# Performance work log

Hardware: AMD Instinct MI355X
Metric: run time of the kernel (lower is better)

## Reference

```python
import jax, jax.numpy as jnp
import numpy as np

N_NODES = 50000
N_EDGES = 800000
D_FEAT = 100


def setup_inputs() -> dict:
    key = jax.random.key(0)
    ks = jax.random.split(key, 10)
    s = 0.1
    x = jax.random.normal(ks[0], (N_NODES, D_FEAT), dtype=jnp.float32)
    edge_index = jax.random.randint(ks[1], (2, N_EDGES), 0, N_NODES, dtype=jnp.int32)
    return {
        "x": x,
        "edge_index": edge_index,
        "convW0": jax.random.normal(ks[2], (100, 100), jnp.float32) * s,
        "convb0": jnp.zeros((100,), jnp.float32),
        "convW1": jax.random.normal(ks[3], (100, 100), jnp.float32) * s,
        "convb1": jnp.zeros((100,), jnp.float32),
        "linW0": jax.random.normal(ks[4], (100, 10), jnp.float32) * s,
        "linb0": jnp.zeros((10,), jnp.float32),
        "linW1": jax.random.normal(ks[5], (10, 1), jnp.float32) * s,
        "linb1": jnp.zeros((1,), jnp.float32),
    }


def _gcn_conv(x, W, b, src, dst, n):
    """PyG GCNConv: h = x @ W; out[i] = sum_{(j->i)} d_j^{-1/2} d_i^{-1/2} h[j] + b,
    with self-loops already included in (src, dst)."""
    h = x @ W  # [N, out]
    deg = jax.ops.segment_sum(jnp.ones(src.shape[0], x.dtype), dst, num_segments=n)
    dinv = jnp.where(deg > 0, jax.lax.rsqrt(deg), jnp.zeros_like(deg))
    norm = dinv[src] * dinv[dst]  # [E_tot]
    msg = norm[:, None] * h[src]  # gather [E_tot, out]
    out = jax.ops.segment_sum(msg, dst, num_segments=n)  # scatter-add
    return out + b


def reference(x, edge_index, convW0, convb0, convW1, convb1, linW0, linb0, linW1, linb1):
    n = x.shape[0]
    # global-norm division (x.div(torch.norm(x).detach()))
    nm = jax.lax.stop_gradient(jnp.linalg.norm(x))
    x = x / nm
    # NOTE: original re-assigns x via sklearn SelectKBest(chi2, k=100) on raw data.x;
    # that is non-differentiable data preprocessing, so we assume x already holds the
    # k=100 selected features.
    loops = jnp.arange(n, dtype=edge_index.dtype)
    src = jnp.concatenate([edge_index[0], loops])  # self-loops appended
    dst = jnp.concatenate([edge_index[1], loops])
    x = _gcn_conv(x, convW0, convb0, src, dst, n)
    x = _gcn_conv(x, convW1, convb1, src, dst, n)
    # MLP head: ReLU between layers, no activation after the last (loop breaks)
    x = jax.nn.relu(x @ linW0 + linb0)
    x = x @ linW1 + linb1
    return x.T  # [1, N]
```

## Files before the change

kernel.cpp:

```cpp
#include <hip/hip_runtime.h>

#define NN 50000
#define NE 800000
#define ELLW 64
#define CSTR 16

__device__ __forceinline__ float wredf(float v) {
    #pragma unroll
    for (int o = 32; o > 0; o >>= 1) v += __shfl_down(v, o, 64);
    return v;
}

__global__ __launch_bounds__(256) void k_fill(
    const int* __restrict__ src, const int* __restrict__ dst,
    int* __restrict__ curp, int* __restrict__ ell,
    const float* __restrict__ W0, const float* __restrict__ W1,
    const float* __restrict__ cb0, const float* __restrict__ cb1,
    const float* __restrict__ L0, const float* __restrict__ lb0,
    float* __restrict__ Wz, float* __restrict__ uvec, float* __restrict__ cvec)
{
    int b = blockIdx.x, t = threadIdx.x;
    if (b < 3125) {
        int e = b * 256 + t;
        int s = src[e];
        int d = dst[e];
        int p = atomicAdd(&curp[d * CSTR], 1);
        if (p < ELLW) ell[d * ELLW + p] = s;
        return;
    }
    __shared__ float WA[1000];
    for (int o = t; o < 1000; o += 256) {
        int j = o / 10, m = o % 10;
        float s = 0.f;
        for (int k = 0; k < 100; ++k) s += W1[j * 100 + k] * L0[k * 10 + m];
        WA[o] = s;
    }
    __syncthreads();
    for (int o = t; o < 1000; o += 256) {
        int i = o / 10, m = o % 10;
        float s = 0.f;
        for (int k = 0; k < 100; ++k) s += W0[i * 100 + k] * WA[k * 10 + m];
        Wz[o] = s;
    }
    if (t < 10) {
        float su = 0.f, scv = 0.f;
        for (int k = 0; k < 100; ++k) {
            su  += cb0[k] * WA[k * 10 + t];
            scv += cb1[k] * L0[k * 10 + t];
        }
        uvec[t] = su;
        cvec[t] = scv + lb0[t];
    }
}

__global__ __launch_bounds__(256) void k_proj(
    const float* __restrict__ x, const float* __restrict__ Wz,
    const int* __restrict__ curp, float* __restrict__ acc,
    float* __restrict__ gp)
{
    __shared__ float w[1000];
    for (int o = threadIdx.x; o < 1000; o += 256) w[o] = Wz[o];
    __syncthreads();
    int i = blockIdx.x * 256 + threadIdx.x;
    float ss = 0.f;
    float h[10];
    #pragma unroll
    for (int m = 0; m < 10; ++m) h[m] = 0.f;
    if (i < NN) {
        const float4* r4 = (const float4*)(x + i * 100);
        for (int kk = 0; kk < 25; ++kk) {
            float4 a = r4[kk];
            ss += a.x * a.x + a.y * a.y + a.z * a.z + a.w * a.w;
            #pragma unroll
            for (int j = 0; j < 4; ++j) {
                float av = ((const float*)&a)[j];
                int k = kk * 4 + j;
                #pragma unroll
                for (int m = 0; m < 10; ++m) h[m] += av * w[k * 10 + m];
            }
        }
    }
    ss = wredf(ss);
    __shared__ float p[4];
    if ((threadIdx.x & 63) == 0) p[threadIdx.x >> 6] = ss;
    __syncthreads();
    if (threadIdx.x == 0) atomicAdd(acc, p[0] + p[1] + p[2] + p[3]);

    if (i < NN) {
        float dv = rsqrtf((float)(curp[i * CSTR] + 1));
        float o16[16];
        #pragma unroll
        for (int m = 0; m < 10; ++m) o16[m] = dv * h[m];
        o16[10] = dv;
        o16[11] = o16[12] = o16[13] = o16[14] = o16[15] = 0.f;
        float4* dst4 = (float4*)(gp + i * 16);
        #pragma unroll
        for (int q = 0; q < 4; ++q) dst4[q] = *(float4*)&o16[q * 4];
    } else if (i == NN) {
        float4 z = {0.f, 0.f, 0.f, 0.f};
        float4* d4 = (float4*)(gp + NN * 16);
        d4[0] = z; d4[1] = z; d4[2] = z; d4[3] = z;
    }
}

__global__ __launch_bounds__(256) void k_agg1(
    const float* __restrict__ gp, const int* __restrict__ curp,
    const int* __restrict__ ell, const float* __restrict__ acc,
    float* __restrict__ tb)
{
    int n = (blockIdx.x * 256 + threadIdx.x) >> 6;
    int l = threadIdx.x & 63, g = l >> 4, lane16 = l & 15;
    if (n > NN) return;
    if (n == NN) {
        if (l < 16) tb[NN * 16 + lane16] = 0.f;
        return;
    }
    int deg = curp[n * CSTR];
    int lim = min(deg, ELLW);
    float dvn = rsqrtf((float)(deg + 1));
    const int* rp = ell + n * ELLW;
    float a0 = (g == 0) ? gp[n * 16 + lane16] : 0.f;
    float a1 = 0.f, a2 = 0.f, a3 = 0.f;
    int nq = (lim + 3) >> 2;
    int k = g, q = 0;
    for (; q + 4 <= nq; q += 4, k += 16) {
        int i0 = (k      < lim) ? rp[k]      : NN;
        int i1 = (k + 4  < lim) ? rp[k + 4]  : NN;
        int i2 = (k + 8  < lim) ? rp[k + 8]  : NN;
        int i3 = (k + 12 < lim) ? rp[k + 12] : NN;
        a0 += gp[i0 * 16 + lane16];
        a1 += gp[i1 * 16 + lane16];
        a2 += gp[i2 * 16 + lane16];
        a3 += gp[i3 * 16 + lane16];
    }
    for (; q < nq; ++q, k += 4) {
        int i0 = (k < lim) ? rp[k] : NN;
        a0 += gp[i0 * 16 + lane16];
    }
    float s = (a0 + a1) + (a2 + a3);
    s += __shfl_xor(s, 16, 64);
    s += __shfl_xor(s, 32, 64);
    if (l < 16) {
        float sc = rsqrtf(*acc);
        float o = (lane16 < 10) ? sc * dvn * dvn * s
                                : (lane16 == 10 ? dvn * s : 0.f);
        tb[n * 16 + lane16] = o;
    }
}

__global__ __launch_bounds__(256) void k_agg2(
    const float* __restrict__ tb, const int* __restrict__ curp,
    const int* __restrict__ ell, const float* __restrict__ uvec,
    const float* __restrict__ cvec, const float* __restrict__ L1,
    const float* __restrict__ lb1, float* __restrict__ out)
{
    __shared__ float su[10], scv[10], sl[10];
    if (threadIdx.x < 10) {
        su[threadIdx.x]  = uvec[threadIdx.x];
        scv[threadIdx.x] = cvec[threadIdx.x];
        sl[threadIdx.x]  = L1[threadIdx.x];
    }
    __syncthreads();
    int n = (blockIdx.x * 256 + threadIdx.x) >> 6;
    int l = threadIdx.x & 63, g = l >> 4, lane16 = l & 15;
    int deg = curp[n * CSTR];
    int lim = min(deg, ELLW);
    float dvn = rsqrtf((float)(deg + 1));
    const int* rp = ell + n * ELLW;
    float a0 = (g == 0) ? tb[n * 16 + lane16] : 0.f;
    float a1 = 0.f, a2 = 0.f, a3 = 0.f;
    int nq = (lim + 3) >> 2;
    int k = g, q = 0;
    for (; q + 4 <= nq; q += 4, k += 16) {
        int i0 = (k      < lim) ? rp[k]      : NN;
        int i1 = (k + 4  < lim) ? rp[k + 4]  : NN;
        int i2 = (k + 8  < lim) ? rp[k + 8]  : NN;
        int i3 = (k + 12 < lim) ? rp[k + 12] : NN;
        a0 += tb[i0 * 16 + lane16];
        a1 += tb[i1 * 16 + lane16];
        a2 += tb[i2 * 16 + lane16];
        a3 += tb[i3 * 16 + lane16];
    }
    for (; q < nq; ++q, k += 4) {
        int i0 = (k < lim) ? rp[k] : NN;
        a0 += tb[i0 * 16 + lane16];
    }
    float s = (a0 + a1) + (a2 + a3);
    s += __shfl_xor(s, 16, 64);
    s += __shfl_xor(s, 32, 64);
    if (l < 16) {
        float v = tb[n * 16 + 10];
        float hidden = 0.f;
        if (lane16 < 10)
            hidden = fmaxf(dvn * s + v * su[lane16] + scv[lane16], 0.f) * sl[lane16];
        #pragma unroll
        for (int o = 8; o; o >>= 1) hidden += __shfl_down(hidden, o, 16);
        if (lane16 == 0) out[n] = hidden + lb1[0];
    }
}

extern "C" void kernel_launch(void* const* d_in, const int* in_sizes, int n_in,
                              void* d_out, int out_size, void* d_ws, size_t ws_size,
                              hipStream_t stream) {
    const float* x   = (const float*)d_in[0];
    const int*   ei  = (const int*)d_in[1];
    const int*   src = ei;
    const int*   dst = ei + NE;
    const float* W0  = (const float*)d_in[2];
    const float* cb0 = (const float*)d_in[3];
    const float* W1  = (const float*)d_in[4];
    const float* cb1 = (const float*)d_in[5];
    const float* lw0 = (const float*)d_in[6];
    const float* lb0 = (const float*)d_in[7];
    const float* lw1 = (const float*)d_in[8];
    const float* lb1 = (const float*)d_in[9];
    float* out = (float*)d_out;

    char* ws = (char*)d_ws;
    float* acc   = (float*)(ws + 0);
    int*   curp  = (int*)  (ws + 256);
    const size_t zspan = 3200384;
    float* Wz    = (float*)(ws + 3200384);
    float* uvec  = (float*)(ws + 3204480);
    float* cvec  = (float*)(ws + 3204608);
    int*   ell   = (int*)  (ws + 3204864);
    float* gp    = (float*)(ws + 16004864);
    float* tb    = (float*)(ws + 19204928);

    hipMemsetAsync(d_ws, 0, zspan, stream);
    k_fill <<<3126, 256, 0, stream>>>(src, dst, curp, ell,
                                      W0, W1, cb0, cb1, lw0, lb0, Wz, uvec, cvec);
    k_proj <<<196, 256, 0, stream>>>(x, Wz, curp, acc, gp);
    k_agg1 <<<12501, 256, 0, stream>>>(gp, curp, ell, acc, tb);
    k_agg2 <<<12500, 256, 0, stream>>>(tb, curp, ell, uvec, cvec, lw1, lb1, out);
}
```

Measured before the change: 211.2 us.

## Pack degree counters densely and broadcast ELL row via wave shuffles

Stores the per-node degree counters contiguously instead of padded at a 64-byte stride, which shrinks the memset span and the counter footprint read by later kernels. In both aggregation kernels each lane loads one ELL entry up front with a coalesced read, and neighbour indices are distributed with __shfl instead of repeated scattered loads from the row. The risk is more atomic contention on shared cache lines during the fill, plus extra cross-lane shuffle instructions.

```diff
diff --git a/kernel.cpp b/kernel.cpp
--- a/kernel.cpp
+++ b/kernel.cpp
@@ -3,7 +3,6 @@
 #define NN 50000
 #define NE 800000
 #define ELLW 64
-#define CSTR 16
 
 __device__ __forceinline__ float wredf(float v) {
     #pragma unroll
@@ -13,7 +12,7 @@
 
 __global__ __launch_bounds__(256) void k_fill(
     const int* __restrict__ src, const int* __restrict__ dst,
-    int* __restrict__ curp, int* __restrict__ ell,
+    int* __restrict__ cursor, int* __restrict__ ell,
     const float* __restrict__ W0, const float* __restrict__ W1,
     const float* __restrict__ cb0, const float* __restrict__ cb1,
     const float* __restrict__ L0, const float* __restrict__ lb0,
@@ -24,7 +23,7 @@
         int e = b * 256 + t;
         int s = src[e];
         int d = dst[e];
-        int p = atomicAdd(&curp[d * CSTR], 1);
+        int p = atomicAdd(&cursor[d], 1);
         if (p < ELLW) ell[d * ELLW + p] = s;
         return;
     }
@@ -55,7 +54,7 @@
 
 __global__ __launch_bounds__(256) void k_proj(
     const float* __restrict__ x, const float* __restrict__ Wz,
-    const int* __restrict__ curp, float* __restrict__ acc,
+    const int* __restrict__ cursor, float* __restrict__ acc,
     float* __restrict__ gp)
 {
     __shared__ float w[1000];
@@ -87,7 +86,7 @@
     if (threadIdx.x == 0) atomicAdd(acc, p[0] + p[1] + p[2] + p[3]);
 
     if (i < NN) {
-        float dv = rsqrtf((float)(curp[i * CSTR] + 1));
+        float dv = rsqrtf((float)(cursor[i] + 1));
         float o16[16];
         #pragma unroll
         for (int m = 0; m < 10; ++m) o16[m] = dv * h[m];
@@ -104,7 +103,7 @@
 }
 
 __global__ __launch_bounds__(256) void k_agg1(
-    const float* __restrict__ gp, const int* __restrict__ curp,
+    const float* __restrict__ gp, const int* __restrict__ cursor,
     const int* __restrict__ ell, const float* __restrict__ acc,
     float* __restrict__ tb)
 {
@@ -115,26 +114,33 @@
         if (l < 16) tb[NN * 16 + lane16] = 0.f;
         return;
     }
-    int deg = curp[n * CSTR];
+    int rpl = ell[n * ELLW + l];
+    int deg = cursor[n];
     int lim = min(deg, ELLW);
     float dvn = rsqrtf((float)(deg + 1));
-    const int* rp = ell + n * ELLW;
     float a0 = (g == 0) ? gp[n * 16 + lane16] : 0.f;
     float a1 = 0.f, a2 = 0.f, a3 = 0.f;
     int nq = (lim + 3) >> 2;
-    int k = g, q = 0;
-    for (; q + 4 <= nq; q += 4, k += 16) {
-        int i0 = (k      < lim) ? rp[k]      : NN;
-        int i1 = (k + 4  < lim) ? rp[k + 4]  : NN;
-        int i2 = (k + 8  < lim) ? rp[k + 8]  : NN;
-        int i3 = (k + 12 < lim) ? rp[k + 12] : NN;
+    int q = 0;
+    for (; q + 4 <= nq; q += 4) {
+        int s0 = 4 * q + g;
+        int v0 = __shfl(rpl, s0,      64);
+        int v1 = __shfl(rpl, s0 + 4,  64);
+        int v2 = __shfl(rpl, s0 + 8,  64);
+        int v3 = __shfl(rpl, s0 + 12, 64);
+        int i0 = (s0      < lim) ? v0 : NN;
+        int i1 = (s0 + 4  < lim) ? v1 : NN;
+        int i2 = (s0 + 8  < lim) ? v2 : NN;
+        int i3 = (s0 + 12 < lim) ? v3 : NN;
         a0 += gp[i0 * 16 + lane16];
         a1 += gp[i1 * 16 + lane16];
         a2 += gp[i2 * 16 + lane16];
         a3 += gp[i3 * 16 + lane16];
     }
-    for (; q < nq; ++q, k += 4) {
-        int i0 = (k < lim) ? rp[k] : NN;
+    for (; q < nq; ++q) {
+        int s0 = 4 * q + g;
+        int v0 = __shfl(rpl, s0, 64);
+        int i0 = (s0 < lim) ? v0 : NN;
         a0 += gp[i0 * 16 + lane16];
     }
     float s = (a0 + a1) + (a2 + a3);
@@ -149,7 +155,7 @@
 }
 
 __global__ __launch_bounds__(256) void k_agg2(
-    const float* __restrict__ tb, const int* __restrict__ curp,
+    const float* __restrict__ tb, const int* __restrict__ cursor,
     const int* __restrict__ ell, const float* __restrict__ uvec,
     const float* __restrict__ cvec, const float* __restrict__ L1,
     const float* __restrict__ lb1, float* __restrict__ out)
@@ -163,26 +169,33 @@
     __syncthreads();
     int n = (blockIdx.x * 256 + threadIdx.x) >> 6;
     int l = threadIdx.x & 63, g = l >> 4, lane16 = l & 15;
-    int deg = curp[n * CSTR];
+    int rpl = ell[n * ELLW + l];
+    int deg = cursor[n];
     int lim = min(deg, ELLW);
     float dvn = rsqrtf((float)(deg + 1));
-    const int* rp = ell + n * ELLW;
     float a0 = (g == 0) ? tb[n * 16 + lane16] : 0.f;
     float a1 = 0.f, a2 = 0.f, a3 = 0.f;
     int nq = (lim + 3) >> 2;
-    int k = g, q = 0;
-    for (; q + 4 <= nq; q += 4, k += 16) {
-        int i0 = (k      < lim) ? rp[k]      : NN;
-        int i1 = (k + 4  < lim) ? rp[k + 4]  : NN;
-        int i2 = (k + 8  < lim) ? rp[k + 8]  : NN;
-        int i3 = (k + 12 < lim) ? rp[k + 12] : NN;
+    int q = 0;
+    for (; q + 4 <= nq; q += 4) {
+        int s0 = 4 * q + g;
+        int v0 = __shfl(rpl, s0,      64);
+        int v1 = __shfl(rpl, s0 + 4,  64);
+        int v2 = __shfl(rpl, s0 + 8,  64);
+        int v3 = __shfl(rpl, s0 + 12, 64);
+        int i0 = (s0      < lim) ? v0 : NN;
+        int i1 = (s0 + 4  < lim) ? v1 : NN;
+        int i2 = (s0 + 8  < lim) ? v2 : NN;
+        int i3 = (s0 + 12 < lim) ? v3 : NN;
         a0 += tb[i0 * 16 + lane16];
         a1 += tb[i1 * 16 + lane16];
         a2 += tb[i2 * 16 + lane16];
         a3 += tb[i3 * 16 + lane16];
     }
-    for (; q < nq; ++q, k += 4) {
-        int i0 = (k < lim) ? rp[k] : NN;
+    for (; q < nq; ++q) {
+        int s0 = 4 * q + g;
+        int v0 = __shfl(rpl, s0, 64);
+        int i0 = (s0 < lim) ? v0 : NN;
         a0 += tb[i0 * 16 + lane16];
     }
     float s = (a0 + a1) + (a2 + a3);
@@ -218,19 +231,19 @@
 
     char* ws = (char*)d_ws;
     float* acc   = (float*)(ws + 0);
-    int*   curp  = (int*)  (ws + 256);
-    const size_t zspan = 3200384;
-    float* Wz    = (float*)(ws + 3200384);
-    float* uvec  = (float*)(ws + 3204480);
-    float* cvec  = (float*)(ws + 3204608);
-    int*   ell   = (int*)  (ws + 3204864);
-    float* gp    = (float*)(ws + 16004864);
-    float* tb    = (float*)(ws + 19204928);
+    int*   cursor= (int*)  (ws + 256);
+    const size_t zspan = 200320;
+    float* Wz    = (float*)(ws + 200448);
+    float* uvec  = (float*)(ws + 204544);
+    float* cvec  = (float*)(ws + 204672);
+    int*   ell   = (int*)  (ws + 204800);
+    float* gp    = (float*)(ws + 13004800);
+    float* tb    = (float*)(ws + 16204864);
 
     hipMemsetAsync(d_ws, 0, zspan, stream);
-    k_fill <<<3126, 256, 0, stream>>>(src, dst, curp, ell,
+    k_fill <<<3126, 256, 0, stream>>>(src, dst, cursor, ell,
                                       W0, W1, cb0, cb1, lw0, lb0, Wz, uvec, cvec);
-    k_proj <<<196, 256, 0, stream>>>(x, Wz, curp, acc, gp);
-    k_agg1 <<<12501, 256, 0, stream>>>(gp, curp, ell, acc, tb);
-    k_agg2 <<<12500, 256, 0, stream>>>(tb, curp, ell, uvec, cvec, lw1, lb1, out);
-}
+    k_proj <<<196, 256, 0, stream>>>(x, Wz, cursor, acc, gp);
+    k_agg1 <<<12501, 256, 0, stream>>>(gp, cursor, ell, acc, tb);
+    k_agg2 <<<12500, 256, 0, stream>>>(tb, cursor, ell, uvec, cvec, lw1, lb1, out);
+}
```

After: 196.6 us. 1.07x faster.
